# Optimization experiments

Measured on AMD Instinct MI355X. Metric: run time of the kernel, lower is better.

Reference implementation:

```python
import math
import jax, jax.numpy as jnp
import numpy as np

B, S, H, D = 2, 2048, 16, 64

def setup_inputs() -> dict:
    key = jax.random.key(0)
    qkv = jax.random.normal(key, (B, S, 3, H, D), dtype=jnp.float32)
    return {"qkv": qkv}

def reference(qkv) -> jnp.ndarray:
    # qkv: [B, S, 3, H, D]
    q = qkv[:, :, 0]  # [B, S, H, D]
    k = qkv[:, :, 1]
    v = qkv[:, :, 2]
    seqlen = qkv.shape[1]
    softmax_scale = 1.0 / math.sqrt(q.shape[-1])
    # scores: [B, H, T, S]
    scores = jnp.einsum('bthd,bshd->bhts', q, k * softmax_scale)
    # additive causal mask with -10000 above the diagonal (matches torch.triu(..., 1))
    causal_mask = jnp.triu(jnp.full((seqlen, seqlen), -10000.0, dtype=scores.dtype), 1)
    scores = scores + causal_mask
    attention = jax.nn.softmax(scores, axis=-1)
    # dropout_p = 0.0 (eval), so no dropout applied
    output = jnp.einsum('bhts,bshd->bthd', attention, v)  # [B, T, H, D]
    return output
```

## Files before the change

### kernel.cpp

```cpp
#include <hip/hip_runtime.h>

typedef __bf16 bf16x8 __attribute__((ext_vector_type(8)));
typedef float f32x4 __attribute__((ext_vector_type(4)));
typedef float f32x16 __attribute__((ext_vector_type(16)));
typedef unsigned int u32;
typedef u32 u32x4 __attribute__((ext_vector_type(4)));

constexpr int Bc = 2, Sc = 2048, Hc = 16, Dc = 64;
constexpr int QBLK = 64, KVBLK = 64;
constexpr int NT = Sc / QBLK;
constexpr int ROWSTR = 3 * Hc * Dc;
constexpr float QSCALE = 0.125f * 1.4426950408889634f;


template <int CTRL>
static __device__ __forceinline__ float dppf(float x) {
  int xi = __builtin_bit_cast(int, x);
  return __builtin_bit_cast(float,
      __builtin_amdgcn_update_dpp(xi, xi, CTRL, 0xF, 0xF, false));
}

static __device__ __forceinline__ u32 pack2(float a, float b) {
  unsigned short x = __builtin_bit_cast(unsigned short, (__bf16)a);
  unsigned short y = __builtin_bit_cast(unsigned short, (__bf16)b);
  return (u32)x | ((u32)y << 16);
}

__global__ __launch_bounds__(256, 2)
void fattn_kernel(const float* __restrict__ qkv, float* __restrict__ out) {
  const int id = blockIdx.x + blockIdx.y * gridDim.x;
  const int swz = (id & 7) * 64 + (id >> 3);
  const int xlow = swz & 15;
  const int xhigh = NT - 1 - xlow;
  const int bh = swz >> 4;
  const int b = bh >> 4, h = bh & 15;

  const int tid = threadIdx.x;
  const int wave = tid >> 6;
  const int lane = tid & 63;
  const int hh = lane >> 5;
  const int q = lane & 31;

  const int myx = (wave < 2) ? xhigh : xlow;
  const int qw = myx * QBLK + (wave & 1) * 32;
  const int myq = qw + q;

  const float* qp = qkv + (size_t)b * Sc * ROWSTR + h * Dc;
  const float* kp = qp + Hc * Dc;
  const float* vp = qp + 2 * Hc * Dc;

  __shared__ __align__(16) char k_s[KVBLK * Dc * 2];
  __shared__ __align__(16) char v_s[Dc * KVBLK * 2];

  bf16x8 qf[4];
#pragma unroll
  for (int c = 0; c < 4; ++c) {
    const float* qr = qp + (size_t)myq * ROWSTR + 16 * c + 8 * hh;
    f32x4 a0 = *(const f32x4*)qr;
    f32x4 a1 = *(const f32x4*)(qr + 4);
    bf16x8 qa;
#pragma unroll
    for (int j = 0; j < 4; ++j) {
      qa[j] = (__bf16)(a0[j] * QSCALE); qa[j + 4] = (__bf16)(a1[j] * QSCALE);
    }
    qf[c] = qa;
  }

  f32x16 o0, o1;
#pragma unroll
  for (int i = 0; i < 16; ++i) { o0[i] = 0.f; o1[i] = 0.f; }
  float mreg = -1e30f, lsum = 0.f;

  const int swq = (q & 7) << 4;

  for (int t = 0; t <= xhigh; ++t) {
    const int kv0 = t * KVBLK;

#pragma unroll
    for (int it = 0; it < 2; ++it) {
      const int u = tid + it * 256, r = u >> 3, g = u & 7;
      const float* ks = kp + (size_t)(kv0 + r) * ROWSTR + g * 8;
      const float* vs = vp + (size_t)(kv0 + r) * ROWSTR + g * 8;
      f32x4 k0 = *(const f32x4*)ks;
      f32x4 k1 = *(const f32x4*)(ks + 4);
      f32x4 v0 = *(const f32x4*)vs;
      f32x4 v1 = *(const f32x4*)(vs + 4);
      bf16x8 kb;
#pragma unroll
      for (int j = 0; j < 4; ++j) { kb[j] = (__bf16)k0[j]; kb[j + 4] = (__bf16)k1[j]; }
      *(bf16x8*)(k_s + ((r * 128 + g * 16) ^ ((r & 7) << 4))) = kb;

      const int odd = r & 1;
      f32x4 tmp = odd ? v0 : v1;
      f32x4 rcv;
#pragma unroll
      for (int j = 0; j < 4; ++j) rcv[j] = dppf<0x128>(tmp[j]);
      const int kvb2 = (r & ~1) * 2;
#pragma unroll
      for (int s = 0; s < 4; ++s) {
        const int dj = (s + g) & 3;
        const float lo = odd ? rcv[dj] : v0[dj];
        const float hi = odd ? v1[dj] : rcv[dj];
        const int d = 8 * g + 4 * odd + dj;
        *(u32*)(v_s + ((d * 128 + kvb2) ^ ((d & 7) << 4))) = pack2(lo, hi);
      }
    }
    __syncthreads();

    if (t <= myx) {
      f32x16 p0, p1;
#pragma unroll
      for (int i = 0; i < 16; ++i) { p0[i] = 0.f; p1[i] = 0.f; }
      __builtin_amdgcn_s_setprio(1);
#pragma unroll
      for (int c = 0; c < 4; ++c) {
        const int off = (16 * c + 8 * hh) * 2;
        bf16x8 kf0 = *(const bf16x8*)(k_s + ((q * 128 + off) ^ swq));
        bf16x8 kf1 = *(const bf16x8*)(k_s + (((32 + q) * 128 + off) ^ swq));
        p0 = __builtin_amdgcn_mfma_f32_32x32x16_bf16(kf0, qf[c], p0, 0, 0, 0);
        p1 = __builtin_amdgcn_mfma_f32_32x32x16_bf16(kf1, qf[c], p1, 0, 0, 0);
      }
      __builtin_amdgcn_s_setprio(0);

      if (t == myx) {
#pragma unroll
        for (int r = 0; r < 16; ++r) {
          const int kvl = (r & 3) + 8 * (r >> 2) + 4 * hh;
          if (kv0 + kvl > myq) p0[r] = -1e30f;
          if (kv0 + 32 + kvl > myq) p1[r] = -1e30f;
        }
      }

      float tr[16];
#pragma unroll
      for (int i = 0; i < 16; ++i) tr[i] = fmaxf(p0[i], p1[i]);
#pragma unroll
      for (int s = 8; s > 0; s >>= 1)
#pragma unroll
        for (int i = 0; i < 8; ++i)
          if (i < s) tr[i] = fmaxf(tr[i], tr[i + s]);
      float pm = fmaxf(tr[0], __shfl_xor(tr[0], 32, 64));

      if (__any(pm > mreg + 8.0f)) {
        float mn = fmaxf(mreg, pm);
        float scl = __builtin_exp2f(mreg - mn);
        mreg = mn;
        lsum *= scl;
        o0 *= scl;
        o1 *= scl;
      }

      float s0 = 0.f, s1 = 0.f, s2 = 0.f, s3 = 0.f;
#pragma unroll
      for (int i = 0; i < 16; ++i) {
        p0[i] = __builtin_exp2f(p0[i] - mreg);
        p1[i] = __builtin_exp2f(p1[i] - mreg);
      }
#pragma unroll
      for (int i = 0; i < 4; ++i) {
        s0 += p0[4 * i + 0] + p1[4 * i + 0];
        s1 += p0[4 * i + 1] + p1[4 * i + 1];
        s2 += p0[4 * i + 2] + p1[4 * i + 2];
        s3 += p0[4 * i + 3] + p1[4 * i + 3];
      }
      lsum += (s0 + s1) + (s2 + s3);

      bf16x8 pb[4];
#pragma unroll
      for (int c = 0; c < 4; ++c) {
        const int m0 = 2 * (c & 1);
        const f32x16& P = (c < 2) ? p0 : p1;
        u32 A0 = pack2(P[4 * m0 + 0], P[4 * m0 + 1]);
        u32 A1 = pack2(P[4 * m0 + 2], P[4 * m0 + 3]);
        u32 B0 = pack2(P[4 * m0 + 4], P[4 * m0 + 5]);
        u32 B1 = pack2(P[4 * m0 + 6], P[4 * m0 + 7]);
        u32 snd0 = hh ? A0 : B0;
        u32 snd1 = hh ? A1 : B1;
        u32 rcv0 = (u32)__shfl_xor((int)snd0, 32, 64);
        u32 rcv1 = (u32)__shfl_xor((int)snd1, 32, 64);
        u32x4 f;
        f[0] = hh ? rcv0 : A0;
        f[1] = hh ? rcv1 : A1;
        f[2] = hh ? B0 : rcv0;
        f[3] = hh ? B1 : rcv1;
        pb[c] = __builtin_bit_cast(bf16x8, f);
      }

      __builtin_amdgcn_s_setprio(1);
#pragma unroll
      for (int c = 0; c < 4; ++c) {
        const int off = (16 * c + 8 * hh) * 2;
        bf16x8 vf0 = *(const bf16x8*)(v_s + ((q * 128 + off) ^ swq));
        bf16x8 vf1 = *(const bf16x8*)(v_s + (((32 + q) * 128 + off) ^ swq));
        o0 = __builtin_amdgcn_mfma_f32_32x32x16_bf16(vf0, pb[c], o0, 0, 0, 0);
        o1 = __builtin_amdgcn_mfma_f32_32x32x16_bf16(vf1, pb[c], o1, 0, 0, 0);
      }
      __builtin_amdgcn_s_setprio(0);
    }
    __syncthreads();
  }

  lsum += __shfl_xor(lsum, 32, 64);
  const float inv = 1.0f / lsum;
  float* op = out + ((size_t)(b * Sc + myq) * Hc + h) * Dc;
#pragma unroll
  for (int m = 0; m < 4; ++m) {
    f32x4 w0, w1;
#pragma unroll
    for (int j = 0; j < 4; ++j) {
      w0[j] = o0[4 * m + j] * inv;
      w1[j] = o1[4 * m + j] * inv;
    }
    const int d0 = 8 * m + 4 * hh;
    *(f32x4*)(op + d0) = w0;
    *(f32x4*)(op + 32 + d0) = w1;
  }
}

extern "C" void kernel_launch(void* const* d_in, const int* in_sizes, int n_in,
                              void* d_out, int out_size, void* d_ws, size_t ws_size,
                              hipStream_t stream) {
  const float* qkv = (const float*)d_in[0];
  float* out = (float*)d_out;
  dim3 grid(NT / 2, Bc * Hc);
  fattn_kernel<<<grid, 256, 0, stream>>>(qkv, out);
}
```

Baseline: 98.65 us.

## Double-buffer K/V shared tiles and prefetch next block into registers

Splits the K/V shared-memory tiles into two buffers. The global loads for the next KV block are issued before computing on the current block, and they are converted and written to the other buffer after the compute. This hides global-load latency behind the MFMA and softmax work and removes one barrier per iteration. In exchange it doubles LDS use to 32KB per block and keeps 32 extra VGPRs live across the compute, which may reduce occupancy under the launch bound of 2 blocks.

After: 97.00 us. About the same (-1.7%).

```diff
diff --git a/kernel.cpp b/kernel.cpp
--- a/kernel.cpp
+++ b/kernel.cpp
@@ -49,8 +49,8 @@
   const float* kp = qp + Hc * Dc;
   const float* vp = qp + 2 * Hc * Dc;
 
-  __shared__ __align__(16) char k_s[KVBLK * Dc * 2];
-  __shared__ __align__(16) char v_s[Dc * KVBLK * 2];
+  __shared__ __align__(16) char k_s[2][KVBLK * Dc * 2];
+  __shared__ __align__(16) char v_s[2][Dc * KVBLK * 2];
 
   bf16x8 qf[4];
 #pragma unroll
@@ -73,41 +73,62 @@
 
   const int swq = (q & 7) << 4;
 
+  const int r_a = tid >> 3, g_a = tid & 7;
+  const int r_b = r_a + 32;
+  f32x4 sk0a, sk1a, sv0a, sv1a, sk0b, sk1b, sv0b, sv1b;
+
+  auto load_kv = [&](int kv0) {
+    const float* ksa = kp + (size_t)(kv0 + r_a) * ROWSTR + g_a * 8;
+    const float* vsa = vp + (size_t)(kv0 + r_a) * ROWSTR + g_a * 8;
+    sk0a = *(const f32x4*)ksa; sk1a = *(const f32x4*)(ksa + 4);
+    sv0a = *(const f32x4*)vsa; sv1a = *(const f32x4*)(vsa + 4);
+    const float* ksb = kp + (size_t)(kv0 + r_b) * ROWSTR + g_a * 8;
+    const float* vsb = vp + (size_t)(kv0 + r_b) * ROWSTR + g_a * 8;
+    sk0b = *(const f32x4*)ksb; sk1b = *(const f32x4*)(ksb + 4);
+    sv0b = *(const f32x4*)vsb; sv1b = *(const f32x4*)(vsb + 4);
+  };
+
+  auto write_unit = [&](char* kd, char* vd, int r, int g,
+                        f32x4 k0, f32x4 k1, f32x4 v0, f32x4 v1) {
+    bf16x8 kb;
+#pragma unroll
+    for (int j = 0; j < 4; ++j) { kb[j] = (__bf16)k0[j]; kb[j + 4] = (__bf16)k1[j]; }
+    *(bf16x8*)(kd + ((r * 128 + g * 16) ^ ((r & 7) << 4))) = kb;
+
+    const int odd = r & 1;
+    f32x4 tmp = odd ? v0 : v1;
+    f32x4 rcv;
+#pragma unroll
+    for (int j = 0; j < 4; ++j) rcv[j] = dppf<0x128>(tmp[j]);
+    const int kvb2 = (r & ~1) * 2;
+#pragma unroll
+    for (int s = 0; s < 4; ++s) {
+      const int dj = (s + g) & 3;
+      const float lo = odd ? rcv[dj] : v0[dj];
+      const float hi = odd ? v1[dj] : rcv[dj];
+      const int d = 8 * g + 4 * odd + dj;
+      *(u32*)(vd + ((d * 128 + kvb2) ^ ((d & 7) << 4))) = pack2(lo, hi);
+    }
+  };
+  auto write_kv = [&](char* kd, char* vd) {
+    write_unit(kd, vd, r_a, g_a, sk0a, sk1a, sv0a, sv1a);
+    write_unit(kd, vd, r_b, g_a, sk0b, sk1b, sv0b, sv1b);
+  };
+
+  load_kv(0);
+  write_kv(k_s[0], v_s[0]);
+  __syncthreads();
+
+  int cur = 0;
   for (int t = 0; t <= xhigh; ++t) {
     const int kv0 = t * KVBLK;
-
-#pragma unroll
-    for (int it = 0; it < 2; ++it) {
-      const int u = tid + it * 256, r = u >> 3, g = u & 7;
-      const float* ks = kp + (size_t)(kv0 + r) * ROWSTR + g * 8;
-      const float* vs = vp + (size_t)(kv0 + r) * ROWSTR + g * 8;
-      f32x4 k0 = *(const f32x4*)ks;
-      f32x4 k1 = *(const f32x4*)(ks + 4);
-      f32x4 v0 = *(const f32x4*)vs;
-      f32x4 v1 = *(const f32x4*)(vs + 4);
-      bf16x8 kb;
-#pragma unroll
-      for (int j = 0; j < 4; ++j) { kb[j] = (__bf16)k0[j]; kb[j + 4] = (__bf16)k1[j]; }
-      *(bf16x8*)(k_s + ((r * 128 + g * 16) ^ ((r & 7) << 4))) = kb;
-
-      const int odd = r & 1;
-      f32x4 tmp = odd ? v0 : v1;
-      f32x4 rcv;
-#pragma unroll
-      for (int j = 0; j < 4; ++j) rcv[j] = dppf<0x128>(tmp[j]);
-      const int kvb2 = (r & ~1) * 2;
-#pragma unroll
-      for (int s = 0; s < 4; ++s) {
-        const int dj = (s + g) & 3;
-        const float lo = odd ? rcv[dj] : v0[dj];
-        const float hi = odd ? v1[dj] : rcv[dj];
-        const int d = 8 * g + 4 * odd + dj;
-        *(u32*)(v_s + ((d * 128 + kvb2) ^ ((d & 7) << 4))) = pack2(lo, hi);
-      }
-    }
-    __syncthreads();
+    const bool more = (t < xhigh);
+    if (more) load_kv(kv0 + KVBLK);
 
     if (t <= myx) {
+      const char* ks = k_s[cur];
+      const char* vs = v_s[cur];
+
       f32x16 p0, p1;
 #pragma unroll
       for (int i = 0; i < 16; ++i) { p0[i] = 0.f; p1[i] = 0.f; }
@@ -115,8 +136,8 @@
 #pragma unroll
       for (int c = 0; c < 4; ++c) {
         const int off = (16 * c + 8 * hh) * 2;
-        bf16x8 kf0 = *(const bf16x8*)(k_s + ((q * 128 + off) ^ swq));
-        bf16x8 kf1 = *(const bf16x8*)(k_s + (((32 + q) * 128 + off) ^ swq));
+        bf16x8 kf0 = *(const bf16x8*)(ks + ((q * 128 + off) ^ swq));
+        bf16x8 kf1 = *(const bf16x8*)(ks + (((32 + q) * 128 + off) ^ swq));
         p0 = __builtin_amdgcn_mfma_f32_32x32x16_bf16(kf0, qf[c], p0, 0, 0, 0);
         p1 = __builtin_amdgcn_mfma_f32_32x32x16_bf16(kf1, qf[c], p1, 0, 0, 0);
       }
@@ -190,14 +211,17 @@
 #pragma unroll
       for (int c = 0; c < 4; ++c) {
         const int off = (16 * c + 8 * hh) * 2;
-        bf16x8 vf0 = *(const bf16x8*)(v_s + ((q * 128 + off) ^ swq));
-        bf16x8 vf1 = *(const bf16x8*)(v_s + (((32 + q) * 128 + off) ^ swq));
+        bf16x8 vf0 = *(const bf16x8*)(vs + ((q * 128 + off) ^ swq));
+        bf16x8 vf1 = *(const bf16x8*)(vs + (((32 + q) * 128 + off) ^ swq));
         o0 = __builtin_amdgcn_mfma_f32_32x32x16_bf16(vf0, pb[c], o0, 0, 0, 0);
         o1 = __builtin_amdgcn_mfma_f32_32x32x16_bf16(vf1, pb[c], o1, 0, 0, 0);
       }
       __builtin_amdgcn_s_setprio(0);
     }
+
+    if (more) write_kv(k_s[cur ^ 1], v_s[cur ^ 1]);
     __syncthreads();
+    cur ^= 1;
   }
 
   lsum += __shfl_xor(lsum, 32, 64);
```
